# Kernel tuning notes

Hardware: AMD Instinct MI355X
Metric: run time of the kernel (lower is better)

## Reference

```python
import jax, jax.numpy as jnp
import numpy as np

N, D, W, S = 16384, 256, 64, 8  # utterances, embed dim, attention half-window, speakers


def setup_inputs() -> dict:
    key = jax.random.key(0)
    ks = jax.random.split(key, 8)
    scale = 1.0 / np.sqrt(D)
    return {
        "x": jax.random.normal(ks[0], (N, D), jnp.float32),
        "speaker_ids": jax.random.randint(ks[1], (N,), 0, S, jnp.int32),
        "W_att": jax.random.normal(ks[2], (D, D), jnp.float32) * scale,
        "W_pred": jax.random.normal(ks[3], (D, D), jnp.float32) * scale,
        "W_suc": jax.random.normal(ks[4], (D, D), jnp.float32) * scale,
        "W_same": jax.random.normal(ks[5], (D, D), jnp.float32) * scale,
        "W_diff": jax.random.normal(ks[6], (D, D), jnp.float32) * scale,
    }


def reference(x, speaker_ids, W_att, W_pred, W_suc, W_same, W_diff):
    n = x.shape[0]
    pad = jnp.zeros((W, D), x.dtype)
    # windowed gather: for utterance i, neighbors at offsets [-W, W-1] (2W slots)
    win_idx = jnp.arange(n)[:, None] + jnp.arange(2 * W)[None, :]  # index into padded [N+2W]
    xp = jnp.concatenate([pad, x, pad], axis=0)                    # [N+2W, D]
    windows = xp[win_idx]                                          # [N, 2W, D]
    # raw_attn[i,w] = (edge_att_weights(windows[i,w])) . x[i]
    raw_attn = jnp.einsum("nwd,ed,ne->nw", windows, W_att, x)      # [N, 2W]
    attn = jax.nn.softmax(raw_attn, axis=1)
    # relation masks over the band: j = i + offset
    offs = jnp.arange(2 * W) - W                                   # [-W, W-1]
    j = jnp.arange(n)[:, None] + offs[None, :]                     # [N, 2W]
    valid = (j >= 0) & (j < n)
    jc = jnp.clip(j, 0, n - 1)
    same_spk = speaker_ids[jc] == speaker_ids[:, None]
    masks = [
        valid & (offs >= 0)[None, :],   # pred: edges to current/future within window
        valid & (offs < 0)[None, :],    # suc: edges to past within window
        valid & same_spk,               # same speaker within window
        valid & ~same_spk,              # different speaker within window
    ]
    # relation-specific GCN aggregation: h = sum_r A_r @ (x @ W_r), A_r banded
    h = jnp.zeros_like(x)
    for Wr, m in zip([W_pred, W_suc, W_same, W_diff], masks):
        support = x @ Wr                                           # [N, D]
        sp = jnp.concatenate([pad, support, pad], axis=0)[win_idx]  # [N, 2W, D]
        h = h + jnp.einsum("nw,nwd->nd", attn * m, sp)
    return jax.nn.log_softmax(h, axis=1)
```

## Files before the change

kernel.cpp:

```cpp
#include <hip/hip_runtime.h>
#include <hip/hip_bf16.h>

typedef unsigned short u16;
typedef unsigned int u32;
typedef __attribute__((ext_vector_type(8))) short short8;
typedef __attribute__((ext_vector_type(4))) float floatx4;

#define NU 16384
#define DIM 256
#define AMS 208

#define XHo 0u
#define XLo 4194304u
#define XRo 8388608u
#define YHo 12582912u
#define YLo 16777216u
#define ST0 20971520u
#define STROW 16512u
#define STMAT 4227072u
#define WH0o 33652736u
#define WL0o 33718272u
#define WRo  33783808u

__device__ __forceinline__ u16 bfh(float v) {
  return (u16)(__float_as_uint(v) >> 16);
}
__device__ __forceinline__ float bup(u16 u) {
  return __uint_as_float(((u32)u) << 16);
}
__device__ __forceinline__ u16 bfrn(float v) {
  u32 u = __float_as_uint(v);
  return (u16)((u + 0x7fffu + ((u >> 16) & 1u)) >> 16);
}

__global__ __launch_bounds__(256) void xprep(const float* __restrict__ x,
                                             u16* __restrict__ ws) {
  int idx = (blockIdx.x * 256 + threadIdx.x) * 8;
  float4 v0 = *(const float4*)(x + idx);
  float4 v1 = *(const float4*)(x + idx + 4);
  float a[8] = {v0.x, v0.y, v0.z, v0.w, v1.x, v1.y, v1.z, v1.w};
  u16 h[8], l[8], r[8];
#pragma unroll
  for (int q = 0; q < 8; ++q) {
    h[q] = bfh(a[q]);
    l[q] = bfh(a[q] - bup(h[q]));
    r[q] = bfrn(a[q]);
  }
  *(uint4*)(ws + XHo + idx) = *(const uint4*)h;
  *(uint4*)(ws + XLo + idx) = *(const uint4*)l;
  *(uint4*)(ws + XRo + idx) = *(const uint4*)r;
}

__global__ __launch_bounds__(256) void wpgz(
    const float* __restrict__ wat, const float* __restrict__ wpr,
    const float* __restrict__ wsu, const float* __restrict__ wsm,
    const float* __restrict__ wdf, u16* __restrict__ ws) {
  const int b = blockIdx.x, t = threadIdx.x;
  if (b < 32) {
    const int s = b & 7, mat = b >> 3, n = t;
    const float* Wa = (mat == 0) ? wat : (mat == 1) ? wpr : (mat == 2) ? wsm : wsu;
    const float* Wb = (mat == 0) ? wat : (mat == 1) ? wsu : (mat == 2) ? wdf : wdf;
    const float c1  = (mat == 0) ? 0.f : (mat == 3) ? 1.f : -1.f;
    u16 hbuf[32], lbuf[32];
#pragma unroll 8
    for (int k = 0; k < 32; ++k) {
      float v = Wa[(s * 32 + k) * 256 + n] + c1 * Wb[(s * 32 + k) * 256 + n];
      if (mat == 0) { hbuf[k] = bfh(v); lbuf[k] = bfh(v - bup(hbuf[k])); }
      else          { hbuf[k] = bfrn(v); }
    }
    u16* dh = ws + ((mat == 0) ? WH0o : (WRo + (size_t)(mat - 1) * 65536))
               + (size_t)s * 8192 + n * 32;
#pragma unroll
    for (int p = 0; p < 4; ++p) *(uint4*)(dh + p * 8) = ((const uint4*)hbuf)[p];
    if (mat == 0) {
      u16* dl = ws + WL0o + (size_t)s * 8192 + n * 32;
#pragma unroll
      for (int p = 0; p < 4; ++p) *(uint4*)(dl + p * 8) = ((const uint4*)lbuf)[p];
    }
  } else {
    int g = (b - 32) * 256 + t;
    int r = g >> 13, rem = g & 8191;
    int d = rem >> 5, p = rem & 31;
    size_t base = ST0 + (size_t)r * STMAT + (size_t)d * STROW;
    size_t off = (p < 16) ? (base + p * 4) : (base + 16448 + (p - 16) * 4);
    *(ushort4*)(ws + off) = make_ushort4(0, 0, 0, 0);
  }
}

__global__ __launch_bounds__(512) void gemmS(u16* __restrict__ ws) {
  __shared__ __align__(16) u16 U[37888];

  const int t = threadIdx.x, path = blockIdx.y, row0 = blockIdx.x * 64;
  const int w = t >> 6, ln = t & 15, quad = (t & 63) >> 4, q8 = quad * 8;
  const int n0 = w * 32;

  if (path == 0) {
#pragma unroll
    for (int cc = 0; cc < 8; ++cc) {
      int idx = t + 512 * cc;
      int buf = idx >> 11, e = idx & 2047;
      int row = e >> 5, c8 = (e & 31) * 8;
      *(uint4*)(U + buf * 16896 + row * 264 + c8) =
          *(const uint4*)(ws + (buf ? XLo : XHo) + (size_t)(row0 + row) * 256 + c8);
    }
    __syncthreads();

    floatx4 acc[4][2];
#pragma unroll
    for (int m = 0; m < 4; ++m)
#pragma unroll
      for (int nt = 0; nt < 2; ++nt) acc[m][nt] = (floatx4){0.f, 0.f, 0.f, 0.f};

    for (int s = 0; s < 8; ++s) {
      short8 ah[4], al[4];
#pragma unroll
      for (int m = 0; m < 4; ++m) {
        ah[m] = *(const short8*)(U + (m * 16 + ln) * 264 + s * 32 + q8);
        al[m] = *(const short8*)(U + 16896 + (m * 16 + ln) * 264 + s * 32 + q8);
      }
      short8 bh[2], bl[2];
#pragma unroll
      for (int nt = 0; nt < 2; ++nt) {
        size_t off = (size_t)s * 8192 + (n0 + nt * 16 + ln) * 32 + q8;
        bh[nt] = *(const short8*)(ws + WH0o + off);
        bl[nt] = *(const short8*)(ws + WL0o + off);
      }
#pragma unroll
      for (int m = 0; m < 4; ++m)
#pragma unroll
        for (int nt = 0; nt < 2; ++nt) {
          acc[m][nt] = __builtin_amdgcn_mfma_f32_16x16x32_bf16(ah[m], bh[nt], acc[m][nt], 0, 0, 0);
          acc[m][nt] = __builtin_amdgcn_mfma_f32_16x16x32_bf16(ah[m], bl[nt], acc[m][nt], 0, 0, 0);
          acc[m][nt] = __builtin_amdgcn_mfma_f32_16x16x32_bf16(al[m], bh[nt], acc[m][nt], 0, 0, 0);
        }
    }
#pragma unroll
    for (int m = 0; m < 4; ++m)
#pragma unroll
      for (int nt = 0; nt < 2; ++nt) {
        int col = n0 + nt * 16 + ln;
#pragma unroll
        for (int r = 0; r < 4; ++r) {
          int row = row0 + m * 16 + quad * 4 + r;
          float y = acc[m][nt][r];
          u16 hh = bfh(y);
          ws[YHo + (size_t)row * 256 + col] = hh;
          ws[YLo + (size_t)row * 256 + col] = bfh(y - bup(hh));
        }
      }
  } else {
#pragma unroll
    for (int cc = 0; cc < 4; ++cc) {
      int idx = t + 512 * cc;
      int row = idx >> 5, c8 = (idx & 31) * 8;
      *(uint4*)(U + row * 264 + c8) =
          *(const uint4*)(ws + XRo + (size_t)(row0 + row) * 256 + c8);
    }
    __syncthreads();

    for (int mat = 0; mat < 3; ++mat) {
      floatx4 acc[4][2];
#pragma unroll
      for (int m = 0; m < 4; ++m)
#pragma unroll
        for (int nt = 0; nt < 2; ++nt) acc[m][nt] = (floatx4){0.f, 0.f, 0.f, 0.f};
      for (int s = 0; s < 8; ++s) {
        short8 ah[4];
#pragma unroll
        for (int m = 0; m < 4; ++m)
          ah[m] = *(const short8*)(U + (m * 16 + ln) * 264 + s * 32 + q8);
        short8 bh[2];
#pragma unroll
        for (int nt = 0; nt < 2; ++nt)
          bh[nt] = *(const short8*)(ws + WRo + (size_t)mat * 65536
                                    + (size_t)s * 8192 + (n0 + nt * 16 + ln) * 32 + q8);
#pragma unroll
        for (int m = 0; m < 4; ++m)
#pragma unroll
          for (int nt = 0; nt < 2; ++nt)
            acc[m][nt] = __builtin_amdgcn_mfma_f32_16x16x32_bf16(ah[m], bh[nt], acc[m][nt], 0, 0, 0);
      }
      __syncthreads();
#pragma unroll
      for (int m = 0; m < 4; ++m)
#pragma unroll
        for (int nt = 0; nt < 2; ++nt) {
          int col = n0 + nt * 16 + ln;
          ushort4 pk = make_ushort4(bfrn(acc[m][nt][0]), bfrn(acc[m][nt][1]),
                                    bfrn(acc[m][nt][2]), bfrn(acc[m][nt][3]));
          *(ushort4*)(U + 16896 + col * 80 + m * 16 + quad * 4) = pk;
        }
      __syncthreads();
      u16* STm = ws + ST0 + (size_t)mat * STMAT;
#pragma unroll
      for (int cc = 0; cc < 4; ++cc) {
        int c = t + 512 * cc;
        int d = c >> 3, part = c & 7;
        *(uint4*)(STm + (size_t)d * STROW + 64 + row0 + part * 8) =
            *(const uint4*)(U + 16896 + d * 80 + part * 8);
      }
    }
  }
}

__global__ __launch_bounds__(512) void fused_attn(
    const u16* __restrict__ ws, const int* __restrict__ spk,
    float* __restrict__ out)
{
  __shared__ __align__(16) u16 stg[12288];
  __shared__ __align__(16) u16 Am[64 * AMS];
  __shared__ int spkw[192];
  __shared__ float prt[64][2], prs[64][2];
  __shared__ float red[64][8];

  const int t    = threadIdx.x;
  const int w    = t >> 6;
  const int ln   = t & 15;
  const int quad = (t & 63) >> 4;
  const int q8   = quad * 8;
  const int i0   = blockIdx.x * 64;
  const int mw   = w & 3;
  const int half = w >> 2;

  if (t < 192) spkw[t] = spk[min(max(i0 - 64 + t, 0), NU - 1)];

  floatx4 accP[6];
#pragma unroll
  for (int cc = 0; cc < 6; ++cc) accP[cc] = (floatx4){0.f, 0.f, 0.f, 0.f};

  for (int kd = 0; kd < DIM; kd += 32) {
#pragma unroll
    for (int cc = 0; cc < 3; ++cc) {
      int idx = t + 512 * cc;
      int buf = (idx >= 768) ? 1 : 0;
      int e   = idx - buf * 768;
      int row = e >> 2, c8 = (e & 3) * 8;
      int jc  = min(max(i0 + row - 64, 0), NU - 1);
      *(uint4*)(stg + buf * 6144 + row * 32 + c8) =
          *(const uint4*)(ws + (buf ? XLo : XHo) + (size_t)jc * 256 + kd + c8);
    }
    __syncthreads();

    size_t yo = (size_t)(i0 + mw * 16 + ln) * 256 + kd + q8;
    short8 yh8 = *(const short8*)(ws + YHo + yo);
    short8 yl8 = *(const short8*)(ws + YLo + yo);
#pragma unroll
    for (int cc = 0; cc < 6; ++cc) {
      int xrow = half * 96 + cc * 16 + ln;
      short8 xbh = *(const short8*)(stg + xrow * 32 + q8);
      short8 xbl = *(const short8*)(stg + 6144 + xrow * 32 + q8);
      accP[cc] = __builtin_amdgcn_mfma_f32_16x16x32_bf16(yh8, xbh, accP[cc], 0, 0, 0);
      accP[cc] = __builtin_amdgcn_mfma_f32_16x16x32_bf16(yh8, xbl, accP[cc], 0, 0, 0);
      accP[cc] = __builtin_amdgcn_mfma_f32_16x16x32_bf16(yl8, xbh, accP[cc], 0, 0, 0);
    }
    __syncthreads();
  }

  int  c_of[6];
  bool vj[6];
#pragma unroll
  for (int cc = 0; cc < 6; ++cc) {
    c_of[cc] = half * 96 + cc * 16 + ln;
    int j = i0 + c_of[cc] - 64;
    vj[cc] = (j >= 0) && (j < NU);
  }
#pragma unroll
  for (int r = 0; r < 4; ++r) {
    int row = mw * 16 + quad * 4 + r;
    float mx = -3.4e38f;
#pragma unroll
    for (int cc = 0; cc < 6; ++cc) {
      int rel = c_of[cc] - row;
      bool inb = (rel >= 0) && (rel < 128);
      if (inb) mx = fmaxf(mx, vj[cc] ? accP[cc][r] : 0.f);
    }
#pragma unroll
    for (int o = 1; o < 16; o <<= 1) mx = fmaxf(mx, __shfl_xor(mx, o));
    if (ln == 0) prt[row][half] = mx;
  }
  __syncthreads();
#pragma unroll
  for (int r = 0; r < 4; ++r) {
    int row = mw * 16 + quad * 4 + r;
    float gm = fmaxf(prt[row][0], prt[row][1]);
    float s = 0.f;
#pragma unroll
    for (int cc = 0; cc < 6; ++cc) {
      int rel = c_of[cc] - row;
      bool inb = (rel >= 0) && (rel < 128);
      float vv = vj[cc] ? accP[cc][r] : 0.f;
      float e  = inb ? __expf(vv - gm) : 0.f;
      s += e;
      accP[cc][r] = (inb && vj[cc]) ? e : 0.f;
    }
#pragma unroll
    for (int o = 1; o < 16; o <<= 1) s += __shfl_xor(s, o);
    if (ln == 0) prs[row][half] = s;
  }
  __syncthreads();
#pragma unroll
  for (int r = 0; r < 4; ++r) {
    int row = mw * 16 + quad * 4 + r;
    float inv = 1.f / (prs[row][0] + prs[row][1]);
#pragma unroll
    for (int cc = 0; cc < 6; ++cc)
      Am[row * AMS + c_of[cc]] = bfrn(accP[cc][r] * inv);
  }
  __syncthreads();

  const int n0 = w * 32;
  floatx4 acc2[4][2];
#pragma unroll
  for (int m = 0; m < 4; ++m)
#pragma unroll
    for (int nt = 0; nt < 2; ++nt) acc2[m][nt] = (floatx4){0.f, 0.f, 0.f, 0.f};

  const int arow = t >> 3, aseg = t & 7;
  const int sr = spkw[arow + 64];

  for (int kj = 0; kj < 192; kj += 32) {
    {
      u16 b0[4], b1[4], b2[4];
#pragma unroll
      for (int q = 0; q < 4; ++q) {
        int c = kj + aseg * 4 + q;
        u16 a = Am[arow * AMS + c];
        b0[q] = (c - arow >= 64) ? a : (u16)0;
        b1[q] = (spkw[c] == sr) ? a : (u16)0;
        b2[q] = a;
      }
      *(ushort4*)(stg + (0 * 64 + arow) * 32 + aseg * 4) = *(const ushort4*)b0;
      *(ushort4*)(stg + (2048 + arow * 32) + aseg * 4)   = *(const ushort4*)b1;
      *(ushort4*)(stg + (4096 + arow * 32) + aseg * 4)   = *(const ushort4*)b2;
    }
    __syncthreads();

#pragma unroll
    for (int rel = 0; rel < 3; ++rel) {
      short8 af[4];
#pragma unroll
      for (int m = 0; m < 4; ++m)
        af[m] = *(const short8*)(stg + rel * 2048 + (m * 16 + ln) * 32 + q8);
#pragma unroll
      for (int nt = 0; nt < 2; ++nt) {
        size_t so = (size_t)ST0 + (size_t)rel * STMAT
                  + (size_t)(n0 + nt * 16 + ln) * STROW + (i0 + kj) + q8;
        short8 bf8 = *(const short8*)(ws + so);
#pragma unroll
        for (int m = 0; m < 4; ++m)
          acc2[m][nt] = __builtin_amdgcn_mfma_f32_16x16x32_bf16(af[m], bf8, acc2[m][nt], 0, 0, 0);
      }
    }
    __syncthreads();
  }

#pragma unroll
  for (int m = 0; m < 4; ++m)
#pragma unroll
    for (int r = 0; r < 4; ++r) {
      float v = fmaxf(acc2[m][0][r], acc2[m][1][r]);
#pragma unroll
      for (int o = 1; o < 16; o <<= 1) v = fmaxf(v, __shfl_xor(v, o));
      if (ln == 0) red[m * 16 + quad * 4 + r][w] = v;
    }
  __syncthreads();
  float gmx[4][4];
#pragma unroll
  for (int m = 0; m < 4; ++m)
#pragma unroll
    for (int r = 0; r < 4; ++r) {
      int row = m * 16 + quad * 4 + r;
      float g = red[row][0];
#pragma unroll
      for (int ww = 1; ww < 8; ++ww) g = fmaxf(g, red[row][ww]);
      gmx[m][r] = g;
    }
  __syncthreads();
#pragma unroll
  for (int m = 0; m < 4; ++m)
#pragma unroll
    for (int r = 0; r < 4; ++r) {
      float e = __expf(acc2[m][0][r] - gmx[m][r]) + __expf(acc2[m][1][r] - gmx[m][r]);
#pragma unroll
      for (int o = 1; o < 16; o <<= 1) e += __shfl_xor(e, o);
      if (ln == 0) red[m * 16 + quad * 4 + r][w] = e;
    }
  __syncthreads();
#pragma unroll
  for (int m = 0; m < 4; ++m)
#pragma unroll
    for (int r = 0; r < 4; ++r) {
      int row = m * 16 + quad * 4 + r;
      float s = red[row][0];
#pragma unroll
      for (int ww = 1; ww < 8; ++ww) s += red[row][ww];
      float lse = gmx[m][r] + logf(s);
      size_t rowg = (size_t)(i0 + row) * DIM;
      out[rowg + n0 + ln]      = acc2[m][0][r] - lse;
      out[rowg + n0 + 16 + ln] = acc2[m][1][r] - lse;
    }
}

extern "C" void kernel_launch(void* const* d_in, const int* in_sizes, int n_in,
                              void* d_out, int out_size, void* d_ws, size_t ws_size,
                              hipStream_t stream) {
  const float* x   = (const float*)d_in[0];
  const int*   spk = (const int*)d_in[1];
  const float* wat = (const float*)d_in[2];
  const float* wpr = (const float*)d_in[3];
  const float* wsu = (const float*)d_in[4];
  const float* wsm = (const float*)d_in[5];
  const float* wdf = (const float*)d_in[6];
  float* out = (float*)d_out;
  u16* ws = (u16*)d_ws;

  hipLaunchKernelGGL(xprep, dim3(2048), dim3(256), 0, stream, x, ws);
  hipLaunchKernelGGL(wpgz, dim3(128), dim3(256), 0, stream,
                     wat, wpr, wsu, wsm, wdf, ws);
  hipLaunchKernelGGL(gemmS, dim3(256, 2), dim3(512), 0, stream, ws);
  hipLaunchKernelGGL(fused_attn, dim3(256), dim3(512), 0, stream, ws, spk, out);
}
```

Before: 154.4 us.

## Double-buffer attention score staging with direct global-to-LDS loads and swizzle

Restructures the fused_attn kernel's score GEMM to double-buffer X tiles in LDS using global_load_lds with an XOR swizzle to avoid bank conflicts, preloading all Y fragments into registers. The masked attention matrices for the aggregation stage are built once into a larger LDS buffer instead of per k-step, removing per-iteration syncs. Block indices are swizzled across the grid to change cache locality. It costs more LDS (lower occupancy) and more registers for the preloaded Y fragments.

```diff
diff --git a/kernel.cpp b/kernel.cpp
--- a/kernel.cpp
+++ b/kernel.cpp
@@ -9,6 +9,8 @@
 #define NU 16384
 #define DIM 256
 #define AMS 208
+#define ACS 200
+#define ACM 12800
 
 #define XHo 0u
 #define XLo 4194304u
@@ -31,6 +33,12 @@
 __device__ __forceinline__ u16 bfrn(float v) {
   u32 u = __float_as_uint(v);
   return (u16)((u + 0x7fffu + ((u >> 16) & 1u)) >> 16);
+}
+
+__device__ __forceinline__ void gload16(const u16* g, u16* l) {
+  __builtin_amdgcn_global_load_lds(
+      (__attribute__((address_space(1))) void*)(uintptr_t)g,
+      (__attribute__((address_space(3))) void*)(uintptr_t)l, 16, 0, 0);
 }
 
 __global__ __launch_bounds__(256) void xprep(const float* __restrict__ x,
@@ -207,7 +215,7 @@
     const u16* __restrict__ ws, const int* __restrict__ spk,
     float* __restrict__ out)
 {
-  __shared__ __align__(16) u16 stg[12288];
+  __shared__ __align__(16) u16 big[38400];
   __shared__ __align__(16) u16 Am[64 * AMS];
   __shared__ int spkw[192];
   __shared__ float prt[64][2], prs[64][2];
@@ -218,40 +226,60 @@
   const int ln   = t & 15;
   const int quad = (t & 63) >> 4;
   const int q8   = quad * 8;
-  const int i0   = blockIdx.x * 64;
+  const int bswz = (blockIdx.x & 7) * 32 + (blockIdx.x >> 3);
+  const int i0   = bswz * 64;
   const int mw   = w & 3;
   const int half = w >> 2;
 
   if (t < 192) spkw[t] = spk[min(max(i0 - 64 + t, 0), NU - 1)];
 
+  auto STAGE = [&](int ks, int par) {
+    const int kd = ks * 32;
+    u16* db = big + par * 12288;
+#pragma unroll
+    for (int cc = 0; cc < 3; ++cc) {
+      int idx  = t + 512 * cc;
+      int bsel = (idx >= 768) ? 1 : 0;
+      int e    = idx - bsel * 768;
+      int row  = e >> 2, s = e & 3;
+      int sw   = s ^ ((row >> 1) & 3);
+      int jc   = min(max(i0 + row - 64, 0), NU - 1);
+      const u16* src = ws + (bsel ? XLo : XHo) + (size_t)jc * 256 + kd + sw * 8;
+      u16* dst = db + bsel * 6144 + e * 8;
+      gload16(src, dst);
+    }
+  };
+
+  short8 yhv[8], ylv[8];
+  {
+    const size_t yb = (size_t)(i0 + mw * 16 + ln) * 256 + q8;
+#pragma unroll
+    for (int ks = 0; ks < 8; ++ks) {
+      yhv[ks] = *(const short8*)(ws + YHo + yb + ks * 32);
+      ylv[ks] = *(const short8*)(ws + YLo + yb + ks * 32);
+    }
+  }
+
   floatx4 accP[6];
 #pragma unroll
   for (int cc = 0; cc < 6; ++cc) accP[cc] = (floatx4){0.f, 0.f, 0.f, 0.f};
 
-  for (int kd = 0; kd < DIM; kd += 32) {
-#pragma unroll
-    for (int cc = 0; cc < 3; ++cc) {
-      int idx = t + 512 * cc;
-      int buf = (idx >= 768) ? 1 : 0;
-      int e   = idx - buf * 768;
-      int row = e >> 2, c8 = (e & 3) * 8;
-      int jc  = min(max(i0 + row - 64, 0), NU - 1);
-      *(uint4*)(stg + buf * 6144 + row * 32 + c8) =
-          *(const uint4*)(ws + (buf ? XLo : XHo) + (size_t)jc * 256 + kd + c8);
-    }
-    __syncthreads();
-
-    size_t yo = (size_t)(i0 + mw * 16 + ln) * 256 + kd + q8;
-    short8 yh8 = *(const short8*)(ws + YHo + yo);
-    short8 yl8 = *(const short8*)(ws + YLo + yo);
+  STAGE(0, 0);
+  __syncthreads();
+#pragma unroll
+  for (int ks = 0; ks < 8; ++ks) {
+    if (ks < 7) STAGE(ks + 1, (ks + 1) & 1);
+    const u16* sp = big + (ks & 1) * 12288;
 #pragma unroll
     for (int cc = 0; cc < 6; ++cc) {
       int xrow = half * 96 + cc * 16 + ln;
-      short8 xbh = *(const short8*)(stg + xrow * 32 + q8);
-      short8 xbl = *(const short8*)(stg + 6144 + xrow * 32 + q8);
-      accP[cc] = __builtin_amdgcn_mfma_f32_16x16x32_bf16(yh8, xbh, accP[cc], 0, 0, 0);
-      accP[cc] = __builtin_amdgcn_mfma_f32_16x16x32_bf16(yh8, xbl, accP[cc], 0, 0, 0);
-      accP[cc] = __builtin_amdgcn_mfma_f32_16x16x32_bf16(yl8, xbh, accP[cc], 0, 0, 0);
+      int slot = quad ^ ((xrow >> 1) & 3);
+      const u16* xb = sp + xrow * 32 + slot * 8;
+      short8 xbh = *(const short8*)xb;
+      short8 xbl = *(const short8*)(xb + 6144);
+      accP[cc] = __builtin_amdgcn_mfma_f32_16x16x32_bf16(yhv[ks], xbh, accP[cc], 0, 0, 0);
+      accP[cc] = __builtin_amdgcn_mfma_f32_16x16x32_bf16(yhv[ks], xbl, accP[cc], 0, 0, 0);
+      accP[cc] = __builtin_amdgcn_mfma_f32_16x16x32_bf16(ylv[ks], xbh, accP[cc], 0, 0, 0);
     }
     __syncthreads();
   }
@@ -308,6 +336,29 @@
   }
   __syncthreads();
 
+  {
+    const int arow = t >> 3, aseg = t & 7;
+    const int sr = spkw[arow + 64];
+#pragma unroll
+    for (int c6 = 0; c6 < 6; ++c6) {
+      int cb = c6 * 32 + aseg * 4;
+      ushort4 av = *(const ushort4*)(Am + arow * AMS + cb);
+      u16 aq[4] = {av.x, av.y, av.z, av.w};
+      u16 b0[4], b1[4], b2[4];
+#pragma unroll
+      for (int q = 0; q < 4; ++q) {
+        int c = cb + q;
+        b0[q] = (c - arow >= 64) ? aq[q] : (u16)0;
+        b1[q] = (spkw[c] == sr) ? aq[q] : (u16)0;
+        b2[q] = aq[q];
+      }
+      *(ushort4*)(big + 0 * ACM + arow * ACS + cb) = *(const ushort4*)b0;
+      *(ushort4*)(big + 1 * ACM + arow * ACS + cb) = *(const ushort4*)b1;
+      *(ushort4*)(big + 2 * ACM + arow * ACS + cb) = *(const ushort4*)b2;
+    }
+  }
+  __syncthreads();
+
   const int n0 = w * 32;
   floatx4 acc2[4][2];
 #pragma unroll
@@ -315,43 +366,23 @@
 #pragma unroll
     for (int nt = 0; nt < 2; ++nt) acc2[m][nt] = (floatx4){0.f, 0.f, 0.f, 0.f};
 
-  const int arow = t >> 3, aseg = t & 7;
-  const int sr = spkw[arow + 64];
-
   for (int kj = 0; kj < 192; kj += 32) {
-    {
-      u16 b0[4], b1[4], b2[4];
-#pragma unroll
-      for (int q = 0; q < 4; ++q) {
-        int c = kj + aseg * 4 + q;
-        u16 a = Am[arow * AMS + c];
-        b0[q] = (c - arow >= 64) ? a : (u16)0;
-        b1[q] = (spkw[c] == sr) ? a : (u16)0;
-        b2[q] = a;
-      }
-      *(ushort4*)(stg + (0 * 64 + arow) * 32 + aseg * 4) = *(const ushort4*)b0;
-      *(ushort4*)(stg + (2048 + arow * 32) + aseg * 4)   = *(const ushort4*)b1;
-      *(ushort4*)(stg + (4096 + arow * 32) + aseg * 4)   = *(const ushort4*)b2;
-    }
-    __syncthreads();
-
 #pragma unroll
     for (int rel = 0; rel < 3; ++rel) {
       short8 af[4];
 #pragma unroll
       for (int m = 0; m < 4; ++m)
-        af[m] = *(const short8*)(stg + rel * 2048 + (m * 16 + ln) * 32 + q8);
+        af[m] = *(const short8*)(big + rel * ACM + (m * 16 + ln) * ACS + kj + q8);
 #pragma unroll
       for (int nt = 0; nt < 2; ++nt) {
         size_t so = (size_t)ST0 + (size_t)rel * STMAT
-                  + (size_t)(n0 + nt * 16 + ln) * STROW + (i0 + kj) + q8;
+                  + (size_t)(n0 + nt * 16 + ln) * STROW + (size_t)(i0 + kj) + q8;
         short8 bf8 = *(const short8*)(ws + so);
 #pragma unroll
         for (int m = 0; m < 4; ++m)
           acc2[m][nt] = __builtin_amdgcn_mfma_f32_16x16x32_bf16(af[m], bf8, acc2[m][nt], 0, 0, 0);
       }
     }
-    __syncthreads();
   }
 
 #pragma unroll
```

New measurement: 147.4 us. -4.6%, faster.
